# Kernel tuning notes

Hardware: AMD Instinct MI355X
Metric: run time of the kernel (lower is better)

## Reference

```python
import jax, jax.numpy as jnp
import numpy as np

F_IN, F_H, N_A, N_B = 256, 512, 40, 4
N_GRAPHS, NODES_PER_GRAPH = 4096, 32
N_NODES = N_GRAPHS * NODES_PER_GRAPH
D_OUT = N_B + N_B * N_A  # 164
BN_EPS = 1e-5


def setup_inputs() -> dict:
    key = jax.random.key(0)
    ks = jax.random.split(key, 8)
    X = jax.random.normal(ks[0], (N_NODES, F_IN), dtype=jnp.float32)
    # fixed-size graphs: consistent NX / NX_rep pair
    NX = jnp.full((N_GRAPHS,), NODES_PER_GRAPH, dtype=jnp.int64)
    NX_rep = jnp.repeat(jnp.arange(N_GRAPHS, dtype=jnp.int64), NODES_PER_GRAPH)
    def kaiming(k, fo, fi):
        return jax.random.normal(k, (fo, fi), dtype=jnp.float32) * np.float32(1.0 / np.sqrt(fi))
    return {
        "X": X, "NX": NX, "NX_rep": NX_rep,
        "W_h": kaiming(ks[1], F_H, 2 * F_IN),          # linear_h (no bias)
        "g_h": jnp.ones((F_H,), jnp.float32), "b_h": jnp.zeros((F_H,), jnp.float32),
        "W_ht": kaiming(ks[2], F_H, F_IN),              # linear_h_t (no bias)
        "g_ht": jnp.ones((F_H,), jnp.float32), "b_ht": jnp.zeros((F_H,), jnp.float32),
        "W_x": kaiming(ks[3], D_OUT, F_H) * 0.1,        # linear_x
        "b_x": jnp.zeros((D_OUT,), jnp.float32),
        "W_xt": kaiming(ks[4], 1, F_H) * 0.1,           # linear_x_t
        "b_xt": jnp.zeros((1,), jnp.float32),
    }


def _batchnorm(x, gamma, beta):
    # BatchNorm1d in training mode: batch statistics, biased variance
    mean = jnp.mean(x, axis=0)
    var = jnp.var(x, axis=0)
    return (x - mean) * jax.lax.rsqrt(var + BN_EPS) * gamma + beta


def reference(X, NX, NX_rep, W_h, g_h, b_h, W_ht, g_ht, b_ht, W_x, b_x, W_xt, b_xt):
    n_graphs = NX.shape[0]
    # graph-level mean pooling via segment sum  -> [G, F_in]
    X_end = jax.ops.segment_sum(X, NX_rep, num_segments=n_graphs) / NX[:, None].astype(X.dtype)
    # concat node features with gathered graph context -> [N, 2*F_in]
    Xc = jnp.concatenate([X, X_end[NX_rep]], axis=1)
    X_h = jax.nn.relu(_batchnorm(Xc @ W_h.T, g_h, b_h))          # [N, F_h]
    X_h_end = jax.nn.relu(_batchnorm(X_end @ W_ht.T, g_ht, b_ht))  # [G, F_h]
    X_x = jnp.exp(X_h @ W_x.T + b_x)                              # [N, D_OUT]
    X_x_end = jnp.exp(X_h_end @ W_xt.T + b_xt)                    # [G, 1]
    # segmented softmax denominator (per graph, over all nodes x D_OUT + end logit)
    X_sum = jnp.sum(jax.ops.segment_sum(X_x, NX_rep, num_segments=n_graphs),
                    axis=-1, keepdims=True) + X_x_end             # [G, 1]
    X_softmax = X_x / X_sum[NX_rep]                               # [N, D_OUT]
    X_softmax_end = X_x_end / X_sum                               # [G, 1]
    connect = X_softmax[:, :N_B]                                  # [N, N_B]
    append = X_softmax[:, N_B:].reshape(-1, N_A, N_B)             # [N, N_A, N_B]
    end = X_softmax_end.squeeze(-1)                               # [G]
    return (append, connect, end)
```

## Files before the change

kernel.cpp:

```cpp
#include <hip/hip_runtime.h>
#include <hip/hip_bf16.h>

typedef __hip_bfloat16 bf16;
typedef __attribute__((ext_vector_type(8))) short bf16x8;
typedef __attribute__((ext_vector_type(4))) float f32x4;

#define N_NODES   131072
#define N_GRAPHS  4096
#define FIN       256
#define FH        512
#define NPAD      176
#define NREAL     164

#define OFF_XB     0UL
#define OFF_XENDB  67108864UL
#define OFF_W1A    69206016UL
#define OFF_BCAT   69468160UL
#define OFF_WXB    69992448UL
#define OFF_STATS  70172672UL
#define OFF_XXE    70180864UL
#define OFF_CCAT   70197248UL
#define OFF_H      86974464UL

__device__ __forceinline__ void gld_lds16(const void* g, void* l) {
  __builtin_amdgcn_global_load_lds(
      (const __attribute__((address_space(1))) void*)g,
      (__attribute__((address_space(3))) void*)l, 16, 0, 0);
}

__device__ __forceinline__ float bf2f(unsigned short u) {
  unsigned int x = ((unsigned int)u) << 16; float f;
  __builtin_memcpy(&f, &x, 4); return f;
}
__device__ __forceinline__ unsigned short f2bf(float f) {
  bf16 h = __float2bfloat16(f); unsigned short u;
  __builtin_memcpy(&u, &h, 2); return u;
}

__global__ __launch_bounds__(256) void k_wcast(
    const float* __restrict__ W_h, const float* __restrict__ W_ht,
    const float* __restrict__ W_x,
    bf16* __restrict__ W1a, bf16* __restrict__ Bcat, bf16* __restrict__ Wxb,
    float* __restrict__ stats)
{
  int i = blockIdx.x * 256 + threadIdx.x;
  if (i < 2048) stats[i] = 0.f;
  if (i < 512 * 512) {
    int of = i >> 9, ic = i & 511;
    float v = W_h[i];
    if (ic < 256) W1a[of * 256 + ic] = __float2bfloat16(v);
    else          Bcat[of * 256 + (ic - 256)] = __float2bfloat16(v);
  }
  if (i < 512 * 256) Bcat[512 * 256 + i] = __float2bfloat16(W_ht[i]);
  if (i < NPAD * 512) {
    int n = i >> 9;
    Wxb[i] = (n < NREAL) ? __float2bfloat16(W_x[i]) : __float2bfloat16(0.f);
  }
}

__global__ __launch_bounds__(256) void k_xend(
    const float* __restrict__ X, const int* __restrict__ NX,
    bf16* __restrict__ Xb, bf16* __restrict__ X_endb)
{
  int g = blockIdx.x;
  int t = threadIdx.x;
  int cg = t & 63;
  int rg = t >> 6;
  const float* Xg = X + (long)g * 32 * FIN;
  bf16* Xbg = Xb + (long)g * 32 * FIN;
  float4 s = {0.f, 0.f, 0.f, 0.f};
  #pragma unroll
  for (int r = 0; r < 8; ++r) {
    int off = (rg * 8 + r) * FIN + cg * 4;
    float4 v = *(const float4*)(Xg + off);
    s.x += v.x; s.y += v.y; s.z += v.z; s.w += v.w;
    ushort4 u = {f2bf(v.x), f2bf(v.y), f2bf(v.z), f2bf(v.w)};
    *(ushort4*)(Xbg + off) = u;
  }
  __shared__ float4 red[256];
  red[t] = s;
  __syncthreads();
  if (t < 64) {
    float4 a = red[t], b = red[t + 64], c = red[t + 128], d = red[t + 192];
    float inv = 1.f / (float)NX[g];
    float4 m = {(a.x + b.x + c.x + d.x) * inv, (a.y + b.y + c.y + d.y) * inv,
                (a.z + b.z + c.z + d.z) * inv, (a.w + b.w + c.w + d.w) * inv};
    ushort4 u = {f2bf(m.x), f2bf(m.y), f2bf(m.z), f2bf(m.w)};
    *(ushort4*)(X_endb + (long)g * FIN + t * 4) = u;
  }
}

__global__ __launch_bounds__(256, 2) void gemm0(
    const bf16* __restrict__ A, const bf16* __restrict__ B,
    float* __restrict__ Cout, float* __restrict__ s1e, float* __restrict__ s2e)
{
  const int bid = blockIdx.x;
  const int blkM = bid >> 3, blkN = bid & 7;
  const int tid = threadIdx.x;
  const int w = tid >> 6, lane = tid & 63;
  const int wm = w >> 1, wn = w & 1;

  __shared__ __align__(16) bf16 lA[128 * 32];
  __shared__ __align__(16) bf16 lB[128 * 32];
  __shared__ float sred[2][2][128];

  f32x4 acc[4][4] = {};
  const int rS = lane >> 2;
  const int cS = (lane & 3) * 8;
  const long baseA = (long)blkM * 128;
  const long baseB = (long)blkN * 128;

  for (int kk = 0; kk < FIN; kk += 32) {
    #pragma unroll
    for (int c = 0; c < 2; ++c) {
      int chunk = 2 * w + c;
      gld_lds16(A + (baseA + chunk * 16 + rS) * FIN + kk + cS, &lA[chunk * 16 * 32]);
      gld_lds16(B + (baseB + chunk * 16 + rS) * FIN + kk + cS, &lB[chunk * 16 * 32]);
    }
    __syncthreads();
    bf16x8 a8[4], b8[4];
    #pragma unroll
    for (int t = 0; t < 4; ++t) {
      a8[t] = *(const bf16x8*)&lA[(wm * 64 + t * 16 + (lane & 15)) * 32 + (lane >> 4) * 8];
      b8[t] = *(const bf16x8*)&lB[(wn * 64 + t * 16 + (lane & 15)) * 32 + (lane >> 4) * 8];
    }
    #pragma unroll
    for (int tm = 0; tm < 4; ++tm)
      #pragma unroll
      for (int tn = 0; tn < 4; ++tn)
        acc[tm][tn] = __builtin_amdgcn_mfma_f32_16x16x32_bf16(a8[tm], b8[tn], acc[tm][tn], 0, 0, 0);
    __syncthreads();
  }

  const int rowq = (lane >> 4) * 4;
  const int coll = lane & 15;
  float p1[4] = {0.f, 0.f, 0.f, 0.f}, p2[4] = {0.f, 0.f, 0.f, 0.f};
  #pragma unroll
  for (int tm = 0; tm < 4; ++tm)
    #pragma unroll
    for (int tn = 0; tn < 4; ++tn)
      #pragma unroll
      for (int r = 0; r < 4; ++r) {
        long row = baseA + wm * 64 + tm * 16 + rowq + r;
        int col = (int)baseB + wn * 64 + tn * 16 + coll;
        float v = acc[tm][tn][r];
        Cout[row * 1024 + col] = v;
        p1[tn] += v; p2[tn] += v * v;
      }

  if (blkN >= 4) {
    #pragma unroll
    for (int tn = 0; tn < 4; ++tn) {
      float q1 = p1[tn], q2 = p2[tn];
      q1 += __shfl_xor(q1, 16); q1 += __shfl_xor(q1, 32);
      q2 += __shfl_xor(q2, 16); q2 += __shfl_xor(q2, 32);
      if (lane < 16) {
        sred[wm][0][wn * 64 + tn * 16 + lane] = q1;
        sred[wm][1][wn * 64 + tn * 16 + lane] = q2;
      }
    }
    __syncthreads();
    int st = tid >> 7, c = tid & 127;
    float v = sred[0][st][c] + sred[1][st][c];
    atomicAdd((st ? s2e : s1e) + (blkN - 4) * 128 + c, v);
  }
}

__global__ __launch_bounds__(256) void k_xxend(
    const float* __restrict__ Ccat, const float* __restrict__ s1e,
    const float* __restrict__ s2e, const float* __restrict__ g_ht,
    const float* __restrict__ b_ht, const float* __restrict__ Wxt,
    const float* __restrict__ bxt, float* __restrict__ Xxe)
{
  __shared__ float aL[512], cL[512];
  int tid = threadIdx.x;
  #pragma unroll
  for (int i = tid; i < 512; i += 256) {
    float mean = s1e[i] * 2.44140625e-4f;
    float var = s2e[i] * 2.44140625e-4f - mean * mean;
    float a = g_ht[i] / sqrtf(var + 1e-5f);
    aL[i] = a; cL[i] = b_ht[i] - mean * a;
  }
  __syncthreads();
  int w = tid >> 6, lane = tid & 63;
  int g = blockIdx.x * 4 + w;
  const float* h = Ccat + (long)g * 1024 + 512;
  float acc = 0.f;
  #pragma unroll
  for (int i = 0; i < 8; ++i) {
    int j = lane + i * 64;
    float x = fmaxf(aL[j] * h[j] + cL[j], 0.f);
    acc += x * Wxt[j];
  }
  #pragma unroll
  for (int off = 32; off; off >>= 1) acc += __shfl_xor(acc, off);
  if (lane == 0) Xxe[g] = expf(acc + bxt[0]);
}

#define G1WAIT(WN) asm volatile("s_waitcnt vmcnt(" #WN ")" ::: "memory");

#define G1S(MTV, KS, WN)                                                       \
  {                                                                            \
    G1WAIT(WN)                                                                 \
    if ((KS) == 0) {                                                           \
      long g0_ = ((long)(MTV)) * 2 + (rowbase >> 5);                           \
      _Pragma("unroll")                                                        \
      for (int a_ = 0; a_ < 2; ++a_)                                           \
        _Pragma("unroll")                                                      \
        for (int j_ = 0; j_ < 4; ++j_)                                         \
          ct[a_][j_] = Ccat[(g0_ + a_) * 1024 + w * 64 + j_ * 16 + coll];      \
    }                                                                          \
    { int tgt_ = (MTV) * 8 + (KS) + 2; if (tgt_ > 63) tgt_ = 63;               \
      const bf16* src_ = Xb + (rowbase + (long)(tgt_ >> 3) * 64 + rS) * FIN    \
                         + (tgt_ & 7) * 32 + cS;                               \
      _Pragma("unroll")                                                        \
      for (int c_ = 0; c_ < 4; ++c_)                                           \
        gld_lds16(src_ + c_ * 16 * FIN, &ring[w][((KS) + 2) & 3][c_ * 512]); } \
    bf16x8 a8_[4];                                                             \
    _Pragma("unroll")                                                          \
    for (int t_ = 0; t_ < 4; ++t_)                                             \
      a8_[t_] = *(const bf16x8*)&ring[w][(KS) & 3][(t_ * 16 + coll) * 32       \
                                                   + hi * 8];                  \
    _Pragma("unroll")                                                          \
    for (int t_ = 0; t_ < 4; ++t_)                                             \
      _Pragma("unroll")                                                        \
      for (int j_ = 0; j_ < 4; ++j_)                                           \
        acc[t_][j_] = __builtin_amdgcn_mfma_f32_16x16x32_bf16(                 \
            a8_[t_], b8[j_][KS], acc[t_][j_], 0, 0, 0);                        \
  }

__global__ __launch_bounds__(512, 2) void gemm1(
    const bf16* __restrict__ Xb, const bf16* __restrict__ W1a,
    const float* __restrict__ Ccat, bf16* __restrict__ H,
    float* __restrict__ s1m, float* __restrict__ s2m)
{
  const int bid = blockIdx.x;
  const int tid = threadIdx.x;
  const int w = tid >> 6, lane = tid & 63;
  const int rS = lane >> 2;
  const int cS = (lane & 3) * 8;
  const int hi = lane >> 4;
  const int coll = lane & 15;

  __shared__ __align__(16) bf16 ring[8][4][2048];

  bf16x8 b8[4][8];
  #pragma unroll
  for (int j = 0; j < 4; ++j)
    #pragma unroll
    for (int ks = 0; ks < 8; ++ks)
      b8[j][ks] = *(const bf16x8*)(W1a + (w * 64 + j * 16 + coll) * FIN
                                   + ks * 32 + hi * 8);

  const long rowbase = (long)bid * 512;
  #pragma unroll
  for (int s = 0; s < 2; ++s)
    #pragma unroll
    for (int c = 0; c < 4; ++c)
      gld_lds16(Xb + (rowbase + c * 16 + rS) * FIN + s * 32 + cS,
                &ring[w][s][c * 512]);

  f32x4 acc[4][4] = {};
  float p1[4] = {0.f, 0.f, 0.f, 0.f}, p2[4] = {0.f, 0.f, 0.f, 0.f};
  float ct[2][4];

  #pragma unroll 1
  for (int mt = 0; mt < 8; ++mt) {
    G1S(mt, 0, 4)  G1S(mt, 1, 12) G1S(mt, 2, 4) G1S(mt, 3, 4)
    G1S(mt, 4, 4)  G1S(mt, 5, 4)  G1S(mt, 6, 4) G1S(mt, 7, 4)

    const long rtile = rowbase + (long)mt * 64;
    #pragma unroll
    for (int t = 0; t < 4; ++t)
      #pragma unroll
      for (int j = 0; j < 4; ++j) {
        int col = w * 64 + j * 16 + coll;
        #pragma unroll
        for (int r = 0; r < 4; ++r) {
          float h = acc[t][j][r] + ct[t >> 1][j];
          H[(rtile + t * 16 + hi * 4 + r) * FH + col] = __float2bfloat16(h);
          p1[j] += h; p2[j] += h * h;
        }
        acc[t][j][0] = 0.f; acc[t][j][1] = 0.f;
        acc[t][j][2] = 0.f; acc[t][j][3] = 0.f;
      }
  }

  #pragma unroll
  for (int j = 0; j < 4; ++j) {
    float q1 = p1[j], q2 = p2[j];
    q1 += __shfl_xor(q1, 16); q1 += __shfl_xor(q1, 32);
    q2 += __shfl_xor(q2, 16); q2 += __shfl_xor(q2, 32);
    if (lane < 16) {
      atomicAdd(s1m + w * 64 + j * 16 + lane, q1);
      atomicAdd(s2m + w * 64 + j * 16 + lane, q2);
    }
  }
}

__global__ __launch_bounds__(256, 2) void gemm2(
    const bf16* __restrict__ Hraw, const bf16* __restrict__ Wxb,
    const float* __restrict__ s1m, const float* __restrict__ s2m,
    const float* __restrict__ g_h, const float* __restrict__ b_h,
    const float* __restrict__ b_x, const float* __restrict__ Xxe,
    float* __restrict__ outA, float* __restrict__ outC, float* __restrict__ outE)
{
  const int blk = blockIdx.x;
  const int tid = threadIdx.x;
  const int w = tid >> 6, lane = tid & 63;

  __shared__ __align__(16) bf16 lA[128 * 32];
  __shared__ __align__(16) bf16 lB[NPAD * 32];
  __shared__ float aL[512], cL[512];

  #pragma unroll
  for (int i = tid; i < 512; i += 256) {
    float mean = s1m[i] * 7.62939453125e-6f;
    float var = s2m[i] * 7.62939453125e-6f - mean * mean;
    float a = g_h[i] / sqrtf(var + 1e-5f);
    aL[i] = a; cL[i] = b_h[i] - mean * a;
  }
  __syncthreads();

  f32x4 acc[2][11] = {};
  const int rS = lane >> 2;
  const int cS = (lane & 3) * 8;
  const long baseRow = (long)blk * 128;

  for (int kk = 0; kk < FH; kk += 32) {
    for (int o = w; o < 11; o += 4)
      gld_lds16(Wxb + (o * 16 + rS) * FH + kk + cS, &lB[o * 16 * 32]);

    f32x4 a0 = *(const f32x4*)&aL[kk + cS];
    f32x4 a1 = *(const f32x4*)&aL[kk + cS + 4];
    f32x4 c0 = *(const f32x4*)&cL[kk + cS];
    f32x4 c1 = *(const f32x4*)&cL[kk + cS + 4];
    #pragma unroll
    for (int c = 0; c < 2; ++c) {
      int chunk = 2 * w + c;
      uint4 raw = *(const uint4*)(Hraw + (baseRow + chunk * 16 + rS) * FH + kk + cS);
      unsigned short* u = (unsigned short*)&raw;
      #pragma unroll
      for (int j = 0; j < 4; ++j) {
        float v = bf2f(u[j]);
        u[j] = f2bf(fmaxf(a0[j] * v + c0[j], 0.f));
      }
      #pragma unroll
      for (int j = 0; j < 4; ++j) {
        float v = bf2f(u[4 + j]);
        u[4 + j] = f2bf(fmaxf(a1[j] * v + c1[j], 0.f));
      }
      *(uint4*)&lA[(chunk * 16 + rS) * 32 + cS] = raw;
    }
    __syncthreads();

    bf16x8 a8[2], b8[11];
    #pragma unroll
    for (int t = 0; t < 2; ++t)
      a8[t] = *(const bf16x8*)&lA[(w * 32 + t * 16 + (lane & 15)) * 32 + (lane >> 4) * 8];
    #pragma unroll
    for (int t = 0; t < 11; ++t)
      b8[t] = *(const bf16x8*)&lB[(t * 16 + (lane & 15)) * 32 + (lane >> 4) * 8];
    #pragma unroll
    for (int tm = 0; tm < 2; ++tm)
      #pragma unroll
      for (int tn = 0; tn < 11; ++tn)
        acc[tm][tn] = __builtin_amdgcn_mfma_f32_16x16x32_bf16(a8[tm], b8[tn], acc[tm][tn], 0, 0, 0);
    __syncthreads();
  }

  const int rowq = (lane >> 4) * 4;
  const int coll = lane & 15;
  const int g = blk * 4 + w;
  float psum = 0.f;
  #pragma unroll
  for (int tn = 0; tn < 11; ++tn) {
    int col = tn * 16 + coll;
    bool valid = col < NREAL;
    float bx = valid ? b_x[col] : 0.f;
    #pragma unroll
    for (int tm = 0; tm < 2; ++tm)
      #pragma unroll
      for (int r = 0; r < 4; ++r) {
        float p = valid ? expf(acc[tm][tn][r] + bx) : 0.f;
        acc[tm][tn][r] = p;
        psum += p;
      }
  }
  #pragma unroll
  for (int off = 32; off; off >>= 1) psum += __shfl_xor(psum, off);
  float Xe = Xxe[g];
  float inv = 1.0f / (psum + Xe);
  if (lane == 0) outE[g] = Xe * inv;

  #pragma unroll
  for (int tn = 0; tn < 11; ++tn) {
    int col = tn * 16 + coll;
    if (col >= NREAL) continue;
    #pragma unroll
    for (int tm = 0; tm < 2; ++tm)
      #pragma unroll
      for (int r = 0; r < 4; ++r) {
        long row = baseRow + w * 32 + tm * 16 + rowq + r;
        float v = acc[tm][tn][r] * inv;
        if (col >= 4) outA[row * 160 + (col - 4)] = v;
        else          outC[row * 4 + col] = v;
      }
  }
}

extern "C" void kernel_launch(void* const* d_in, const int* in_sizes, int n_in,
                              void* d_out, int out_size, void* d_ws, size_t ws_size,
                              hipStream_t stream)
{
  const float* X    = (const float*)d_in[0];
  const int*   NX   = (const int*)d_in[1];
  const float* W_h  = (const float*)d_in[3];
  const float* g_h  = (const float*)d_in[4];
  const float* b_h  = (const float*)d_in[5];
  const float* W_ht = (const float*)d_in[6];
  const float* g_ht = (const float*)d_in[7];
  const float* b_ht = (const float*)d_in[8];
  const float* W_x  = (const float*)d_in[9];
  const float* b_x  = (const float*)d_in[10];
  const float* W_xt = (const float*)d_in[11];
  const float* b_xt = (const float*)d_in[12];

  char* ws = (char*)d_ws;
  bf16*  Xb    = (bf16*)(ws + OFF_XB);
  bf16*  X_endb= (bf16*)(ws + OFF_XENDB);
  bf16*  W1a   = (bf16*)(ws + OFF_W1A);
  bf16*  Bcat  = (bf16*)(ws + OFF_BCAT);
  bf16*  Wxb   = (bf16*)(ws + OFF_WXB);
  float* stats = (float*)(ws + OFF_STATS);
  float* s1m = stats, *s2m = stats + 512, *s1e = stats + 1024, *s2e = stats + 1536;
  float* Xxe   = (float*)(ws + OFF_XXE);
  float* Ccat  = (float*)(ws + OFF_CCAT);
  bf16*  H     = (bf16*)(ws + OFF_H);

  float* outA = (float*)d_out;
  float* outC = outA + (long)N_NODES * 160;
  float* outE = outC + (long)N_NODES * 4;

  k_wcast<<<1024, 256, 0, stream>>>(W_h, W_ht, W_x, W1a, Bcat, Wxb, stats);
  k_xend<<<N_GRAPHS, 256, 0, stream>>>(X, NX, Xb, X_endb);
  gemm0<<<256, 256, 0, stream>>>(X_endb, Bcat, Ccat, s1e, s2e);
  k_xxend<<<1024, 256, 0, stream>>>(Ccat, s1e, s2e, g_ht, b_ht, W_xt, b_xt, Xxe);
  gemm1<<<256, 512, 0, stream>>>(Xb, W1a, Ccat, H, s1m, s2m);
  gemm2<<<1024, 256, 0, stream>>>(H, Wxb, s1m, s2m, g_h, b_h, b_x, Xxe, outA, outC, outE);
}
```

Before: 398.7 us.

## Restructure gemm2 with half-K resident weights and per-wave register-prefetched A tiles

```diff
diff --git a/kernel.cpp b/kernel.cpp
--- a/kernel.cpp
+++ b/kernel.cpp
@@ -211,16 +211,16 @@
           ct[a_][j_] = Ccat[(g0_ + a_) * 1024 + w * 64 + j_ * 16 + coll];      \
     }                                                                          \
     { int tgt_ = (MTV) * 8 + (KS) + 2; if (tgt_ > 63) tgt_ = 63;               \
-      const bf16* src_ = Xb + (rowbase + (long)(tgt_ >> 3) * 64 + rS) * FIN    \
-                         + (tgt_ & 7) * 32 + cS;                               \
+      const bf16* src_ = Xb + (rowbase + (long)(tgt_ >> 3) * 64 + coll) * FIN  \
+                         + (tgt_ & 7) * 32 + hi * 8;                           \
       _Pragma("unroll")                                                        \
       for (int c_ = 0; c_ < 4; ++c_)                                           \
         gld_lds16(src_ + c_ * 16 * FIN, &ring[w][((KS) + 2) & 3][c_ * 512]); } \
     bf16x8 a8_[4];                                                             \
     _Pragma("unroll")                                                          \
     for (int t_ = 0; t_ < 4; ++t_)                                             \
-      a8_[t_] = *(const bf16x8*)&ring[w][(KS) & 3][(t_ * 16 + coll) * 32       \
-                                                   + hi * 8];                  \
+      a8_[t_] = *(const bf16x8*)&ring[w][(KS) & 3][t_ * 512                    \
+                                                   + (hi * 16 + coll) * 8];    \
     _Pragma("unroll")                                                          \
     for (int t_ = 0; t_ < 4; ++t_)                                             \
       _Pragma("unroll")                                                        \
@@ -237,8 +237,6 @@
   const int bid = blockIdx.x;
   const int tid = threadIdx.x;
   const int w = tid >> 6, lane = tid & 63;
-  const int rS = lane >> 2;
-  const int cS = (lane & 3) * 8;
   const int hi = lane >> 4;
   const int coll = lane & 15;
 
@@ -257,7 +255,7 @@
   for (int s = 0; s < 2; ++s)
     #pragma unroll
     for (int c = 0; c < 4; ++c)
-      gld_lds16(Xb + (rowbase + c * 16 + rS) * FIN + s * 32 + cS,
+      gld_lds16(Xb + (rowbase + c * 16 + coll) * FIN + s * 32 + hi * 8,
                 &ring[w][s][c * 512]);
 
   f32x4 acc[4][4] = {};
@@ -298,7 +296,7 @@
   }
 }
 
-__global__ __launch_bounds__(256, 2) void gemm2(
+__global__ __launch_bounds__(512, 2) void gemm2(
     const bf16* __restrict__ Hraw, const bf16* __restrict__ Wxb,
     const float* __restrict__ s1m, const float* __restrict__ s2m,
     const float* __restrict__ g_h, const float* __restrict__ b_h,
@@ -308,70 +306,119 @@
   const int blk = blockIdx.x;
   const int tid = threadIdx.x;
   const int w = tid >> 6, lane = tid & 63;
-
-  __shared__ __align__(16) bf16 lA[128 * 32];
-  __shared__ __align__(16) bf16 lB[NPAD * 32];
-  __shared__ float aL[512], cL[512];
-
-  #pragma unroll
-  for (int i = tid; i < 512; i += 256) {
-    float mean = s1m[i] * 7.62939453125e-6f;
-    float var = s2m[i] * 7.62939453125e-6f - mean * mean;
-    float a = g_h[i] / sqrtf(var + 1e-5f);
-    aL[i] = a; cL[i] = b_h[i] - mean * a;
-  }
-  __syncthreads();
-
-  f32x4 acc[2][11] = {};
   const int rS = lane >> 2;
   const int cS = (lane & 3) * 8;
-  const long baseRow = (long)blk * 128;
-
-  for (int kk = 0; kk < FH; kk += 32) {
-    for (int o = w; o < 11; o += 4)
-      gld_lds16(Wxb + (o * 16 + rS) * FH + kk + cS, &lB[o * 16 * 32]);
-
-    f32x4 a0 = *(const f32x4*)&aL[kk + cS];
-    f32x4 a1 = *(const f32x4*)&aL[kk + cS + 4];
-    f32x4 c0 = *(const f32x4*)&cL[kk + cS];
-    f32x4 c1 = *(const f32x4*)&cL[kk + cS + 4];
-    #pragma unroll
-    for (int c = 0; c < 2; ++c) {
-      int chunk = 2 * w + c;
-      uint4 raw = *(const uint4*)(Hraw + (baseRow + chunk * 16 + rS) * FH + kk + cS);
-      unsigned short* u = (unsigned short*)&raw;
-      #pragma unroll
-      for (int j = 0; j < 4; ++j) {
-        float v = bf2f(u[j]);
-        u[j] = f2bf(fmaxf(a0[j] * v + c0[j], 0.f));
-      }
-      #pragma unroll
-      for (int j = 0; j < 4; ++j) {
-        float v = bf2f(u[4 + j]);
-        u[4 + j] = f2bf(fmaxf(a1[j] * v + c1[j], 0.f));
-      }
-      *(uint4*)&lA[(chunk * 16 + rS) * 32 + cS] = raw;
-    }
-    __syncthreads();
-
-    bf16x8 a8[2], b8[11];
-    #pragma unroll
-    for (int t = 0; t < 2; ++t)
-      a8[t] = *(const bf16x8*)&lA[(w * 32 + t * 16 + (lane & 15)) * 32 + (lane >> 4) * 8];
-    #pragma unroll
-    for (int t = 0; t < 11; ++t)
-      b8[t] = *(const bf16x8*)&lB[(t * 16 + (lane & 15)) * 32 + (lane >> 4) * 8];
-    #pragma unroll
-    for (int tm = 0; tm < 2; ++tm)
-      #pragma unroll
-      for (int tn = 0; tn < 11; ++tn)
-        acc[tm][tn] = __builtin_amdgcn_mfma_f32_16x16x32_bf16(a8[tm], b8[tn], acc[tm][tn], 0, 0, 0);
-    __syncthreads();
-  }
-
-  const int rowq = (lane >> 4) * 4;
+  const int hi = lane >> 4;
   const int coll = lane & 15;
-  const int g = blk * 4 + w;
+
+  __shared__ __align__(16) bf16 lB[88 * 512];
+  __shared__ __align__(16) bf16 lA[8][1024];
+  __shared__ float aL[512], cL[512];
+
+  {
+    float mean = s1m[tid] * 7.62939453125e-6f;
+    float var = s2m[tid] * 7.62939453125e-6f - mean * mean;
+    float a = g_h[tid] / sqrtf(var + 1e-5f);
+    aL[tid] = a; cL[tid] = b_h[tid] - mean * a;
+  }
+
+  #pragma unroll
+  for (int j = 0; j < 11; ++j) {
+    int u = j * 8 + w;
+    int ks = u / 11, o = u - ks * 11;
+    gld_lds16(Wxb + (o * 16 + coll) * FH + ks * 32 + hi * 8, &lB[u * 512]);
+  }
+
+  const long wrow = (long)blk * 256 + w * 32;
+
+  #define G2X(rawv, kof)                                                     \
+    { f32x4 a0_ = *(const f32x4*)&aL[(kof) + cS];                            \
+      f32x4 a1_ = *(const f32x4*)&aL[(kof) + cS + 4];                        \
+      f32x4 c0_ = *(const f32x4*)&cL[(kof) + cS];                            \
+      f32x4 c1_ = *(const f32x4*)&cL[(kof) + cS + 4];                        \
+      unsigned short* u_ = (unsigned short*)&(rawv);                         \
+      _Pragma("unroll")                                                      \
+      for (int q_ = 0; q_ < 4; ++q_) {                                       \
+        float v_ = bf2f(u_[q_]);                                             \
+        u_[q_] = f2bf(fmaxf(a0_[q_] * v_ + c0_[q_], 0.f));                   \
+      }                                                                      \
+      _Pragma("unroll")                                                      \
+      for (int q_ = 0; q_ < 4; ++q_) {                                       \
+        float v_ = bf2f(u_[4 + q_]);                                         \
+        u_[4 + q_] = f2bf(fmaxf(a1_[q_] * v_ + c1_[q_], 0.f));               \
+      }                                                                      \
+    }
+
+  uint4 hA[2], hB[2];
+  __syncthreads();
+  #pragma unroll
+  for (int c = 0; c < 2; ++c) {
+    uint4 raw = *(const uint4*)(Hraw + (wrow + c * 16 + rS) * FH + cS);
+    G2X(raw, 0)
+    *(uint4*)&lA[w][c * 512 + ((lane & 3) * 16 + rS) * 8] = raw;
+  }
+  #pragma unroll
+  for (int c = 0; c < 2; ++c)
+    hA[c] = *(const uint4*)(Hraw + (wrow + c * 16 + rS) * FH + 32 + cS);
+  #pragma unroll
+  for (int c = 0; c < 2; ++c)
+    hB[c] = *(const uint4*)(Hraw + (wrow + c * 16 + rS) * FH + 64 + cS);
+
+  asm volatile("s_waitcnt vmcnt(0)" ::: "memory");
+  __syncthreads();
+
+  f32x4 acc[2][11] = {};
+
+  #pragma unroll 1
+  for (int half = 0; half < 2; ++half) {
+    #pragma unroll
+    for (int ks = 0; ks < 8; ++ks) {
+      const int step = half * 8 + ks;
+      bf16x8 a8[2];
+      #pragma unroll
+      for (int t = 0; t < 2; ++t)
+        a8[t] = *(const bf16x8*)&lA[w][t * 512 + (hi * 16 + coll) * 8];
+      if (step < 15) {
+        #pragma unroll
+        for (int c = 0; c < 2; ++c) {
+          uint4 raw = hA[c];
+          G2X(raw, (step + 1) * 32)
+          *(uint4*)&lA[w][c * 512 + ((lane & 3) * 16 + rS) * 8] = raw;
+        }
+        hA[0] = hB[0]; hA[1] = hB[1];
+        if (step < 13) {
+          #pragma unroll
+          for (int c = 0; c < 2; ++c)
+            hB[c] = *(const uint4*)(Hraw + (wrow + c * 16 + rS) * FH
+                                    + (step + 3) * 32 + cS);
+        }
+      }
+      #pragma unroll
+      for (int tn = 0; tn < 11; ++tn) {
+        bf16x8 bb = *(const bf16x8*)&lB[(ks * 11 + tn) * 512
+                                        + (hi * 16 + coll) * 8];
+        #pragma unroll
+        for (int tm = 0; tm < 2; ++tm)
+          acc[tm][tn] = __builtin_amdgcn_mfma_f32_16x16x32_bf16(
+              a8[tm], bb, acc[tm][tn], 0, 0, 0);
+      }
+    }
+    if (half == 0) {
+      __syncthreads();
+      #pragma unroll
+      for (int j = 0; j < 11; ++j) {
+        int u = j * 8 + w;
+        int ks = u / 11, o = u - ks * 11;
+        gld_lds16(Wxb + (o * 16 + coll) * FH + 256 + ks * 32 + hi * 8,
+                  &lB[u * 512]);
+      }
+      asm volatile("s_waitcnt vmcnt(0)" ::: "memory");
+      __syncthreads();
+    }
+  }
+
+  const int rowq = hi * 4;
+  const int g = blk * 8 + w;
   float psum = 0.f;
   #pragma unroll
   for (int tn = 0; tn < 11; ++tn) {
@@ -401,7 +448,7 @@
     for (int tm = 0; tm < 2; ++tm)
       #pragma unroll
       for (int r = 0; r < 4; ++r) {
-        long row = baseRow + w * 32 + tm * 16 + rowq + r;
+        long row = wrow + tm * 16 + rowq + r;
         float v = acc[tm][tn][r] * inv;
         if (col >= 4) outA[row * 160 + (col - 4)] = v;
         else          outC[row * 4 + col] = v;
@@ -447,5 +494,5 @@
   gemm0<<<256, 256, 0, stream>>>(X_endb, Bcat, Ccat, s1e, s2e);
   k_xxend<<<1024, 256, 0, stream>>>(Ccat, s1e, s2e, g_ht, b_ht, W_xt, b_xt, Xxe);
   gemm1<<<256, 512, 0, stream>>>(Xb, W1a, Ccat, H, s1m, s2m);
-  gemm2<<<1024, 256, 0, stream>>>(H, Wxb, s1m, s2m, g_h, b_h, b_x, Xxe, outA, outC, outE);
-}
+  gemm2<<<512, 512, 0, stream>>>(H, Wxb, s1m, s2m, g_h, b_h, b_x, Xxe, outA, outC, outE);
+}
```

Result: slower. 418.7 us (+5.0%).
